# Kernel optimization log

Measured on AMD Instinct MI355X. Metric: run time of the kernel, lower is better.

Reference implementation:

```python
import jax, jax.numpy as jnp
import numpy as np
import itertools

F = 3          # num_sparse_features
C = 256        # num_categories
D = 64         # embedding_dim
H = 1024       # hidden_units
ND = 13        # num_dense_features
B = 16384      # batch
COMBOS = [c for r in range(2, F + 1) for c in itertools.combinations(range(F), r)]
WIDE_DIM = C * F + sum(C ** len(c) for c in COMBOS) + ND
DEEP_IN = F * D + ND


def setup_inputs() -> dict:
    key = jax.random.key(0)
    ks = jax.random.split(key, 12)
    sparse_inputs = jax.random.randint(ks[0], (B, F), 0, C, dtype=jnp.int32)
    dense_inputs = jax.random.normal(ks[1], (B, ND), dtype=jnp.float32)
    wide_w = jax.random.normal(ks[2], (WIDE_DIM,), dtype=jnp.float32) * 0.01
    wide_b = jax.random.normal(ks[3], (1,), dtype=jnp.float32) * 0.01
    emb = jax.random.normal(ks[4], (F, C, D), dtype=jnp.float32) * 0.05
    W1 = jax.random.normal(ks[5], (H, DEEP_IN), dtype=jnp.float32) / np.sqrt(DEEP_IN).astype(np.float32)
    b1 = jnp.zeros((H,), jnp.float32)
    W2 = jax.random.normal(ks[6], (H, H), dtype=jnp.float32) / np.sqrt(H).astype(np.float32)
    b2 = jnp.zeros((H,), jnp.float32)
    W3 = jax.random.normal(ks[7], (1, H), dtype=jnp.float32) / np.sqrt(H).astype(np.float32)
    b3 = jnp.zeros((1,), jnp.float32)
    return {"sparse_inputs": sparse_inputs, "dense_inputs": dense_inputs,
            "wide_w": wide_w, "wide_b": wide_b, "emb": emb,
            "W1": W1, "b1": b1, "W2": W2, "b2": b2, "W3": W3, "b3": b3}


def reference(sparse_inputs, dense_inputs, wide_w, wide_b, emb, W1, b1, W2, b2, W3, b3):
    # Wide path: one_hot(x) @ W.T  ==  gather of W columns at the hot indices.
    wide = wide_b[0]  # scalar, broadcasts to [B]
    for i in range(F):  # per-feature one-hot block, width C each
        wide = wide + wide_w[i * C + sparse_inputs[:, i]]
    off = F * C
    for combo in COMBOS:  # cross-feature one-hot blocks, width C**len(combo)
        cross = sparse_inputs[:, combo[0]]
        for j in combo[1:]:
            # faithful to source: multiplies by num_sparse_features (F), not C
            cross = cross * F + sparse_inputs[:, j]
        wide = wide + wide_w[off + cross]
        off += C ** len(combo)
    wide = wide + dense_inputs @ wide_w[off:off + ND]  # dense tail of wide linear
    wide = wide[:, None]  # [B, 1]

    # Deep path: per-feature embedding lookup -> concat -> 3-layer MLP
    embedded = jnp.concatenate([emb[i][sparse_inputs[:, i]] for i in range(F)], axis=1)  # [B, F*D]
    deep_x = jnp.concatenate([embedded, dense_inputs], axis=1)  # [B, DEEP_IN]
    h = jax.nn.relu(deep_x @ W1.T + b1)
    h = jax.nn.relu(h @ W2.T + b2)
    deep = h @ W3.T + b3  # [B, 1]

    return jax.nn.sigmoid(wide + deep)
```

## Files before the change

kernel.cpp:

```cpp
#include <hip/hip_runtime.h>
#include <stdint.h>


#define BATCH 16384
#define HDIM 1024
#define KPAD 256
#define DEEP_IN 205

typedef short bf16x8 __attribute__((ext_vector_type(8)));
typedef float f32x4 __attribute__((ext_vector_type(4)));
typedef uint16_t u16x8 __attribute__((ext_vector_type(8)));

__device__ __forceinline__ float bf2f(uint16_t u) {
    uint32_t x = ((uint32_t)u) << 16;
    float f;
    __builtin_memcpy(&f, &x, 4);
    return f;
}

__device__ __forceinline__ uint16_t f2bf(float f) {
    uint32_t x;
    __builtin_memcpy(&x, &f, 4);
    uint32_t r = (x + 0x7fffu + ((x >> 16) & 1u)) >> 16;
    return (uint16_t)r;
}

__device__ __forceinline__ void async_ld16(const uint16_t* g, uint16_t* l) {
    __builtin_amdgcn_global_load_lds(
        (const __attribute__((address_space(1))) uint32_t*)g,
        (__attribute__((address_space(3))) uint32_t*)l, 16, 0, 0);
}

__global__ __launch_bounds__(256) void prep_kernel(
    const int* __restrict__ sp, const float* __restrict__ dense,
    const float* __restrict__ emb,
    const float* __restrict__ W1, const float* __restrict__ W2,
    const float* __restrict__ ww, const float* __restrict__ wb,
    const float* __restrict__ b3,
    uint16_t* __restrict__ dx, uint16_t* __restrict__ W1b,
    uint16_t* __restrict__ W2b, float* __restrict__ wide)
{
    const int bid = blockIdx.x;
    if (bid < 2048) {
        int idx = bid * 256 + threadIdx.x;
        int b = idx >> 5, c0 = (idx & 31) * 8;
        u16x8 o;
        if (c0 < 192) {
            int f = c0 >> 6, cc = c0 & 63;
            int s = sp[b * 3 + f];
            const float* e = emb + (size_t)(((f << 8) + s) * 64 + cc);
            float4 v0 = *(const float4*)e;
            float4 v1 = *(const float4*)(e + 4);
            o[0] = f2bf(v0.x); o[1] = f2bf(v0.y); o[2] = f2bf(v0.z); o[3] = f2bf(v0.w);
            o[4] = f2bf(v1.x); o[5] = f2bf(v1.y); o[6] = f2bf(v1.z); o[7] = f2bf(v1.w);
        } else {
#pragma unroll
            for (int t = 0; t < 8; t++) {
                int c = c0 + t;
                o[t] = (c >= 192 && c < DEEP_IN) ? f2bf(dense[b * 13 + (c - 192)])
                                                 : (uint16_t)0;
            }
        }
        *(u16x8*)(dx + (size_t)idx * 8) = o;
    } else if (bid < 2560) {
        int k = (bid - 2048) * 256 + threadIdx.x;
        const float* src = W2 + (size_t)k * 8;
        float4 v0 = *(const float4*)src;
        float4 v1 = *(const float4*)(src + 4);
        u16x8 o;
        o[0] = f2bf(v0.x); o[1] = f2bf(v0.y); o[2] = f2bf(v0.z); o[3] = f2bf(v0.w);
        o[4] = f2bf(v1.x); o[5] = f2bf(v1.y); o[6] = f2bf(v1.z); o[7] = f2bf(v1.w);
        *(u16x8*)(W2b + (size_t)k * 8) = o;
    } else if (bid < 2688) {
        int idx = (bid - 2560) * 256 + threadIdx.x;
        int n = idx >> 5, c0 = (idx & 31) * 8;
        u16x8 o;
#pragma unroll
        for (int t = 0; t < 8; t++) {
            int c = c0 + t;
            o[t] = (c < DEEP_IN) ? f2bf(W1[n * DEEP_IN + c]) : (uint16_t)0;
        }
        *(u16x8*)(W1b + (size_t)idx * 8) = o;
    } else {
        int b = (bid - 2688) * 256 + threadIdx.x;
        int s0 = sp[b * 3], s1 = sp[b * 3 + 1], s2 = sp[b * 3 + 2];
        float w = wb[0] + b3[0];
        w += ww[s0] + ww[256 + s1] + ww[512 + s2];
        w += ww[768    + s0 * 3 + s1];
        w += ww[66304  + s0 * 3 + s2];
        w += ww[131840 + s1 * 3 + s2];
        w += ww[197376 + (s0 * 3 + s1) * 3 + s2];
        const float* wd = ww + 16974592;
        float acc = 0.f;
#pragma unroll
        for (int j = 0; j < 13; j++) acc += dense[b * 13 + j] * wd[j];
        wide[b] = w + acc;
    }
}

#define GEMM_CORE(A_, B_, K_)                                                  \
    const int tid = threadIdx.x;                                               \
    const int lane = tid & 63;                                                 \
    const int wave = tid >> 6;                                                 \
    const int wm = wave >> 2;                                                  \
    const int wn = wave & 3;                                                   \
    const int id = blockIdx.x;                                                 \
    const int xcd = id & 7;                                                    \
    const int slot = id >> 3;                                                  \
    const int mbX = (M >> 7) >> 3;                                             \
    const int by = xcd * mbX + (slot >> 2);                                    \
    const int bx = slot & 3;                                                   \
    const int bm = by * 128;                                                   \
    const int bn = bx * 256;                                                   \
    const int rl = lane & 15, q = lane >> 4;                                   \
    f32x4 acc[4][4];                                                           \
    _Pragma("unroll") for (int i = 0; i < 4; i++)                              \
        _Pragma("unroll") for (int j = 0; j < 4; j++) acc[i][j] = (f32x4)0.f;  \
    const uint16_t* aS = A_ + (size_t)(bm + wave * 16 + rl) * K_ + q * 8;      \
    const uint16_t* bS0 = B_ + (size_t)(bn + wave * 32 + rl) * K_ + q * 8;     \
    const uint16_t* bS1 = bS0 + (size_t)16 * K_;                               \
    const int dA = wave * 512, dB0 = wave * 1024, dB1 = wave * 1024 + 512;     \
    async_ld16(aS, &Al[0][dA]);                                                \
    async_ld16(bS0, &Bl[0][dB0]);                                              \
    async_ld16(bS1, &Bl[0][dB1]);                                              \
    asm volatile("s_waitcnt vmcnt(0)" ::: "memory");                           \
    __syncthreads();                                                           \
    int p = 0;                                                                 \
    for (int k0 = 32; k0 < K_; k0 += 32) {                                     \
        async_ld16(aS + k0, &Al[p ^ 1][dA]);                                   \
        async_ld16(bS0 + k0, &Bl[p ^ 1][dB0]);                                 \
        async_ld16(bS1 + k0, &Bl[p ^ 1][dB1]);                                 \
        bf16x8 af[4], bfr[4];                                                  \
        _Pragma("unroll") for (int i = 0; i < 4; i++)                          \
            af[i] = *(const bf16x8*)&Al[p][(wm * 4 + i) * 512 + lane * 8];     \
        _Pragma("unroll") for (int j = 0; j < 4; j++)                          \
            bfr[j] = *(const bf16x8*)&Bl[p][(wn * 4 + j) * 512 + lane * 8];    \
        _Pragma("unroll") for (int i = 0; i < 4; i++)                          \
            _Pragma("unroll") for (int j = 0; j < 4; j++)                      \
                acc[i][j] = __builtin_amdgcn_mfma_f32_16x16x32_bf16(           \
                    af[i], bfr[j], acc[i][j], 0, 0, 0);                        \
        asm volatile("s_waitcnt vmcnt(0)" ::: "memory");                       \
        __syncthreads();                                                       \
        p ^= 1;                                                                \
    }                                                                          \
    {                                                                          \
        bf16x8 af[4], bfr[4];                                                  \
        _Pragma("unroll") for (int i = 0; i < 4; i++)                          \
            af[i] = *(const bf16x8*)&Al[p][(wm * 4 + i) * 512 + lane * 8];     \
        _Pragma("unroll") for (int j = 0; j < 4; j++)                          \
            bfr[j] = *(const bf16x8*)&Bl[p][(wn * 4 + j) * 512 + lane * 8];    \
        _Pragma("unroll") for (int i = 0; i < 4; i++)                          \
            _Pragma("unroll") for (int j = 0; j < 4; j++)                      \
                acc[i][j] = __builtin_amdgcn_mfma_f32_16x16x32_bf16(           \
                    af[i], bfr[j], acc[i][j], 0, 0, 0);                        \
    }

__global__ __launch_bounds__(512, 4) void gemm_relu(
    const uint16_t* __restrict__ A, const uint16_t* __restrict__ Bw,
    const float* __restrict__ bias, uint16_t* __restrict__ C,
    int M, int N, int K)
{
    __shared__ __align__(16) uint16_t Al[2][4096];
    __shared__ __align__(16) uint16_t Bl[2][8192];
    GEMM_CORE(A, Bw, K)
#pragma unroll
    for (int i = 0; i < 4; i++) {
#pragma unroll
        for (int j = 0; j < 4; j++) {
            int n = bn + (wn * 4 + j) * 16 + rl;
            float bv = bias[n];
#pragma unroll
            for (int r = 0; r < 4; r++) {
                int m = bm + (wm * 4 + i) * 16 + q * 4 + r;
                float v = fmaxf(acc[i][j][r] + bv, 0.f);
                C[(size_t)m * N + n] = f2bf(v);
            }
        }
    }
}

__global__ __launch_bounds__(512, 4) void gemm_fused(
    const uint16_t* __restrict__ A, const uint16_t* __restrict__ Bw,
    const float* __restrict__ bias, const float* __restrict__ W3,
    float* __restrict__ outacc, int M, int N, int K)
{
    __shared__ __align__(16) uint16_t Al[2][4096];
    __shared__ __align__(16) uint16_t Bl[2][8192];
    GEMM_CORE(A, Bw, K)
    float bv[4], w3v[4];
#pragma unroll
    for (int j = 0; j < 4; j++) {
        int n = bn + (wn * 4 + j) * 16 + rl;
        bv[j] = bias[n];
        w3v[j] = W3[n];
    }
#pragma unroll
    for (int i = 0; i < 4; i++) {
#pragma unroll
        for (int r = 0; r < 4; r++) {
            float pt = 0.f;
#pragma unroll
            for (int j = 0; j < 4; j++)
                pt += fmaxf(acc[i][j][r] + bv[j], 0.f) * w3v[j];
            pt += __shfl_xor(pt, 1);
            pt += __shfl_xor(pt, 2);
            pt += __shfl_xor(pt, 4);
            pt += __shfl_xor(pt, 8);
            if (rl == 0) {
                int m = bm + (wm * 4 + i) * 16 + q * 4 + r;
                atomicAdd(&outacc[m], pt);
            }
        }
    }
}

__global__ __launch_bounds__(256) void sigmoid_kernel(
    const float* __restrict__ outacc, float* __restrict__ out)
{
    int b = blockIdx.x * 256 + threadIdx.x;
    out[b] = 1.f / (1.f + __expf(-outacc[b]));
}

extern "C" void kernel_launch(void* const* d_in, const int* in_sizes, int n_in,
                              void* d_out, int out_size, void* d_ws, size_t ws_size,
                              hipStream_t stream) {
    const int*   sp    = (const int*)d_in[0];
    const float* dense = (const float*)d_in[1];
    const float* ww    = (const float*)d_in[2];
    const float* wb    = (const float*)d_in[3];
    const float* emb   = (const float*)d_in[4];
    const float* W1    = (const float*)d_in[5];
    const float* b1    = (const float*)d_in[6];
    const float* W2    = (const float*)d_in[7];
    const float* b2    = (const float*)d_in[8];
    const float* W3    = (const float*)d_in[9];
    const float* b3    = (const float*)d_in[10];
    float* out = (float*)d_out;

    char* ws = (char*)d_ws;
    float*    wide = (float*)ws;
    uint16_t* dxp  = (uint16_t*)(ws + 65536);
    uint16_t* W1b  = (uint16_t*)(ws + 8454144);
    uint16_t* W2b  = (uint16_t*)(ws + 8978432);
    uint16_t* h1   = (uint16_t*)(ws + 11075584);

    prep_kernel<<<2752, 256, 0, stream>>>(sp, dense, emb, W1, W2, ww, wb, b3,
                                          dxp, W1b, W2b, wide);
    gemm_relu<<<(BATCH / 128) * 4, 512, 0, stream>>>(
        dxp, W1b, b1, h1, BATCH, HDIM, KPAD);
    gemm_fused<<<(BATCH / 128) * 4, 512, 0, stream>>>(
        h1, W2b, b2, W3, wide, BATCH, HDIM, HDIM);
    sigmoid_kernel<<<BATCH / 256, 256, 0, stream>>>(wide, out);
}
```

Before: 184.0 us.

## Switch GEMM core to triple-buffered LDS pipeline with one barrier per step

The GEMM main loop moves from double to triple buffering in shared memory. Each step waits with vmcnt(3), so the next tile's loads stay in flight, and uses a single s_barrier per iteration instead of a full drain plus barrier. Redundant wraparound prefetches are issued at the end so the loop stays uniform. The cost is 50% more LDS per block, which can lower occupancy, plus a few wasted loads in the last iterations.

```diff
diff --git a/kernel.cpp b/kernel.cpp
--- a/kernel.cpp
+++ b/kernel.cpp
@@ -120,48 +120,46 @@
     const uint16_t* bS0 = B_ + (size_t)(bn + wave * 32 + rl) * K_ + q * 8;     \
     const uint16_t* bS1 = bS0 + (size_t)16 * K_;                               \
     const int dA = wave * 512, dB0 = wave * 1024, dB1 = wave * 1024 + 512;     \
+    const int niter = (K_) >> 5;                                               \
+       \
     async_ld16(aS, &Al[0][dA]);                                                \
     async_ld16(bS0, &Bl[0][dB0]);                                              \
     async_ld16(bS1, &Bl[0][dB1]);                                              \
-    asm volatile("s_waitcnt vmcnt(0)" ::: "memory");                           \
-    __syncthreads();                                                           \
-    int p = 0;                                                                 \
-    for (int k0 = 32; k0 < K_; k0 += 32) {                                     \
-        async_ld16(aS + k0, &Al[p ^ 1][dA]);                                   \
-        async_ld16(bS0 + k0, &Bl[p ^ 1][dB0]);                                 \
-        async_ld16(bS1 + k0, &Bl[p ^ 1][dB1]);                                 \
+    async_ld16(aS + 32, &Al[1][dA]);                                           \
+    async_ld16(bS0 + 32, &Bl[1][dB0]);                                         \
+    async_ld16(bS1 + 32, &Bl[1][dB1]);                                         \
+    int pc = 0;                                              \
+    int k2 = 2;                     \
+    if (k2 >= niter) k2 -= niter;                                              \
+    for (int k = 0; k < niter; ++k) {                                          \
+        asm volatile("s_waitcnt vmcnt(3)" ::: "memory");                       \
+        asm volatile("s_barrier" ::: "memory");                                \
+        int pf = pc + 2; if (pf >= 3) pf -= 3;                                 \
+        const int ko = k2 << 5;                                                \
+        async_ld16(aS + ko, &Al[pf][dA]);                                      \
+        async_ld16(bS0 + ko, &Bl[pf][dB0]);                                    \
+        async_ld16(bS1 + ko, &Bl[pf][dB1]);                                    \
+        k2++; if (k2 >= niter) k2 = 0;                                         \
         bf16x8 af[4], bfr[4];                                                  \
         _Pragma("unroll") for (int i = 0; i < 4; i++)                          \
-            af[i] = *(const bf16x8*)&Al[p][(wm * 4 + i) * 512 + lane * 8];     \
+            af[i] = *(const bf16x8*)&Al[pc][(wm * 4 + i) * 512 + lane * 8];    \
         _Pragma("unroll") for (int j = 0; j < 4; j++)                          \
-            bfr[j] = *(const bf16x8*)&Bl[p][(wn * 4 + j) * 512 + lane * 8];    \
+            bfr[j] = *(const bf16x8*)&Bl[pc][(wn * 4 + j) * 512 + lane * 8];   \
         _Pragma("unroll") for (int i = 0; i < 4; i++)                          \
             _Pragma("unroll") for (int j = 0; j < 4; j++)                      \
                 acc[i][j] = __builtin_amdgcn_mfma_f32_16x16x32_bf16(           \
                     af[i], bfr[j], acc[i][j], 0, 0, 0);                        \
-        asm volatile("s_waitcnt vmcnt(0)" ::: "memory");                       \
-        __syncthreads();                                                       \
-        p ^= 1;                                                                \
+        pc++; if (pc >= 3) pc -= 3;                                            \
     }                                                                          \
-    {                                                                          \
-        bf16x8 af[4], bfr[4];                                                  \
-        _Pragma("unroll") for (int i = 0; i < 4; i++)                          \
-            af[i] = *(const bf16x8*)&Al[p][(wm * 4 + i) * 512 + lane * 8];     \
-        _Pragma("unroll") for (int j = 0; j < 4; j++)                          \
-            bfr[j] = *(const bf16x8*)&Bl[p][(wn * 4 + j) * 512 + lane * 8];    \
-        _Pragma("unroll") for (int i = 0; i < 4; i++)                          \
-            _Pragma("unroll") for (int j = 0; j < 4; j++)                      \
-                acc[i][j] = __builtin_amdgcn_mfma_f32_16x16x32_bf16(           \
-                    af[i], bfr[j], acc[i][j], 0, 0, 0);                        \
-    }
+    asm volatile("s_waitcnt vmcnt(0)" ::: "memory");
 
 __global__ __launch_bounds__(512, 4) void gemm_relu(
     const uint16_t* __restrict__ A, const uint16_t* __restrict__ Bw,
     const float* __restrict__ bias, uint16_t* __restrict__ C,
     int M, int N, int K)
 {
-    __shared__ __align__(16) uint16_t Al[2][4096];
-    __shared__ __align__(16) uint16_t Bl[2][8192];
+    __shared__ __align__(16) uint16_t Al[3][4096];
+    __shared__ __align__(16) uint16_t Bl[3][8192];
     GEMM_CORE(A, Bw, K)
 #pragma unroll
     for (int i = 0; i < 4; i++) {
@@ -184,8 +182,8 @@
     const float* __restrict__ bias, const float* __restrict__ W3,
     float* __restrict__ outacc, int M, int N, int K)
 {
-    __shared__ __align__(16) uint16_t Al[2][4096];
-    __shared__ __align__(16) uint16_t Bl[2][8192];
+    __shared__ __align__(16) uint16_t Al[3][4096];
+    __shared__ __align__(16) uint16_t Bl[3][8192];
     GEMM_CORE(A, Bw, K)
     float bv[4], w3v[4];
 #pragma unroll
```

New measurement: 190.0 us. 3.3% more time.

## Switch GEMMs to 32x32x16 MFMA tiles and trim first-layer K padding

Applied to the files above, without the earlier changes.

Replaces the 16x16x32 bf16 MFMA fragments with 32x32x16 MFMAs (2x2 accumulators of 16 floats per wave) and reworks the LDS staging layout and epilogue indexing to match. It also shrinks the padded K of the first layer from 256 to 224, which cuts both prep work and first-GEMM iterations. The larger MFMA gives more FLOPs per LDS fragment read and fewer instructions. The risk lies in the LDS fragment mapping and the output row indexing, which must match the 32x32 accumulator layout exactly.

```diff
diff --git a/kernel.cpp b/kernel.cpp
--- a/kernel.cpp
+++ b/kernel.cpp
@@ -4,19 +4,12 @@
 
 #define BATCH 16384
 #define HDIM 1024
-#define KPAD 256
+#define K1 224
 #define DEEP_IN 205
 
 typedef short bf16x8 __attribute__((ext_vector_type(8)));
-typedef float f32x4 __attribute__((ext_vector_type(4)));
+typedef float f32x16 __attribute__((ext_vector_type(16)));
 typedef uint16_t u16x8 __attribute__((ext_vector_type(8)));
-
-__device__ __forceinline__ float bf2f(uint16_t u) {
-    uint32_t x = ((uint32_t)u) << 16;
-    float f;
-    __builtin_memcpy(&f, &x, 4);
-    return f;
-}
 
 __device__ __forceinline__ uint16_t f2bf(float f) {
     uint32_t x;
@@ -41,9 +34,9 @@
     uint16_t* __restrict__ W2b, float* __restrict__ wide)
 {
     const int bid = blockIdx.x;
-    if (bid < 2048) {
+    if (bid < 1792) {
         int idx = bid * 256 + threadIdx.x;
-        int b = idx >> 5, c0 = (idx & 31) * 8;
+        int b = idx / 28, c0 = (idx - b * 28) * 8;
         u16x8 o;
         if (c0 < 192) {
             int f = c0 >> 6, cc = c0 & 63;
@@ -57,13 +50,13 @@
 #pragma unroll
             for (int t = 0; t < 8; t++) {
                 int c = c0 + t;
-                o[t] = (c >= 192 && c < DEEP_IN) ? f2bf(dense[b * 13 + (c - 192)])
-                                                 : (uint16_t)0;
+                o[t] = (c < DEEP_IN) ? f2bf(dense[b * 13 + (c - 192)])
+                                     : (uint16_t)0;
             }
         }
-        *(u16x8*)(dx + (size_t)idx * 8) = o;
-    } else if (bid < 2560) {
-        int k = (bid - 2048) * 256 + threadIdx.x;
+        *(u16x8*)(dx + (size_t)b * K1 + c0) = o;
+    } else if (bid < 2304) {
+        int k = (bid - 1792) * 256 + threadIdx.x;
         const float* src = W2 + (size_t)k * 8;
         float4 v0 = *(const float4*)src;
         float4 v1 = *(const float4*)(src + 4);
@@ -71,18 +64,18 @@
         o[0] = f2bf(v0.x); o[1] = f2bf(v0.y); o[2] = f2bf(v0.z); o[3] = f2bf(v0.w);
         o[4] = f2bf(v1.x); o[5] = f2bf(v1.y); o[6] = f2bf(v1.z); o[7] = f2bf(v1.w);
         *(u16x8*)(W2b + (size_t)k * 8) = o;
-    } else if (bid < 2688) {
-        int idx = (bid - 2560) * 256 + threadIdx.x;
-        int n = idx >> 5, c0 = (idx & 31) * 8;
+    } else if (bid < 2416) {
+        int idx = (bid - 2304) * 256 + threadIdx.x;
+        int n = idx / 28, c0 = (idx - n * 28) * 8;
         u16x8 o;
 #pragma unroll
         for (int t = 0; t < 8; t++) {
             int c = c0 + t;
             o[t] = (c < DEEP_IN) ? f2bf(W1[n * DEEP_IN + c]) : (uint16_t)0;
         }
-        *(u16x8*)(W1b + (size_t)idx * 8) = o;
+        *(u16x8*)(W1b + (size_t)n * K1 + c0) = o;
     } else {
-        int b = (bid - 2688) * 256 + threadIdx.x;
+        int b = (bid - 2416) * 256 + threadIdx.x;
         int s0 = sp[b * 3], s1 = sp[b * 3 + 1], s2 = sp[b * 3 + 2];
         float w = wb[0] + b3[0];
         w += ww[s0] + ww[256 + s1] + ww[512 + s2];
@@ -112,47 +105,62 @@
     const int bx = slot & 3;                                                   \
     const int bm = by * 128;                                                   \
     const int bn = bx * 256;                                                   \
-    const int rl = lane & 15, q = lane >> 4;                                   \
-    f32x4 acc[4][4];                                                           \
-    _Pragma("unroll") for (int i = 0; i < 4; i++)                              \
-        _Pragma("unroll") for (int j = 0; j < 4; j++) acc[i][j] = (f32x4)0.f;  \
-    const uint16_t* aS = A_ + (size_t)(bm + wave * 16 + rl) * K_ + q * 8;      \
-    const uint16_t* bS0 = B_ + (size_t)(bn + wave * 32 + rl) * K_ + q * 8;     \
-    const uint16_t* bS1 = bS0 + (size_t)16 * K_;                               \
-    const int dA = wave * 512, dB0 = wave * 1024, dB1 = wave * 1024 + 512;     \
+    const int rl32 = lane & 31, q2 = lane >> 5;                                \
+    f32x16 acc[2][2];                                                          \
+    _Pragma("unroll") for (int i = 0; i < 2; i++)                              \
+        _Pragma("unroll") for (int j = 0; j < 2; j++) acc[i][j] = (f32x16)0.f; \
+    const uint16_t* aS = A_ + (size_t)(bm + (wave >> 1) * 32 + rl32) * K_      \
+                            + (wave & 1) * 16 + q2 * 8;                        \
+    const uint16_t* bS = B_ + (size_t)(bn + wave * 32 + rl32) * K_ + q2 * 8;   \
+    const int dA = wave * 512;                                                 \
+    const int dB0 = (2 * wave) * 512, dB1 = (2 * wave + 1) * 512;              \
     async_ld16(aS, &Al[0][dA]);                                                \
-    async_ld16(bS0, &Bl[0][dB0]);                                              \
-    async_ld16(bS1, &Bl[0][dB1]);                                              \
+    async_ld16(bS, &Bl[0][dB0]);                                               \
+    async_ld16(bS + 16, &Bl[0][dB1]);                                          \
     asm volatile("s_waitcnt vmcnt(0)" ::: "memory");                           \
     __syncthreads();                                                           \
     int p = 0;                                                                 \
     for (int k0 = 32; k0 < K_; k0 += 32) {                                     \
         async_ld16(aS + k0, &Al[p ^ 1][dA]);                                   \
-        async_ld16(bS0 + k0, &Bl[p ^ 1][dB0]);                                 \
-        async_ld16(bS1 + k0, &Bl[p ^ 1][dB1]);                                 \
-        bf16x8 af[4], bfr[4];                                                  \
-        _Pragma("unroll") for (int i = 0; i < 4; i++)                          \
-            af[i] = *(const bf16x8*)&Al[p][(wm * 4 + i) * 512 + lane * 8];     \
-        _Pragma("unroll") for (int j = 0; j < 4; j++)                          \
-            bfr[j] = *(const bf16x8*)&Bl[p][(wn * 4 + j) * 512 + lane * 8];    \
-        _Pragma("unroll") for (int i = 0; i < 4; i++)                          \
-            _Pragma("unroll") for (int j = 0; j < 4; j++)                      \
-                acc[i][j] = __builtin_amdgcn_mfma_f32_16x16x32_bf16(           \
-                    af[i], bfr[j], acc[i][j], 0, 0, 0);                        \
+        async_ld16(bS + k0, &Bl[p ^ 1][dB0]);                                  \
+        async_ld16(bS + k0 + 16, &Bl[p ^ 1][dB1]);                             \
+        bf16x8 af[2][2], bfr[2][2];                                            \
+        _Pragma("unroll") for (int i = 0; i < 2; i++)                          \
+            _Pragma("unroll") for (int kc = 0; kc < 2; kc++)                   \
+                af[i][kc] = *(const bf16x8*)                                   \
+                    &Al[p][((wm * 2 + i) * 2 + kc) * 512 + lane * 8];          \
+        _Pragma("unroll") for (int j = 0; j < 2; j++)                          \
+            _Pragma("unroll") for (int kc = 0; kc < 2; kc++)                   \
+                bfr[j][kc] = *(const bf16x8*)                                  \
+                    &Bl[p][((wn * 2 + j) * 2 + kc) * 512 + lane * 8];          \
+        _Pragma("unroll") for (int i = 0; i < 2; i++)                          \
+            _Pragma("unroll") for (int j = 0; j < 2; j++) {                    \
+                acc[i][j] = __builtin_amdgcn_mfma_f32_32x32x16_bf16(           \
+                    af[i][0], bfr[j][0], acc[i][j], 0, 0, 0);                  \
+                acc[i][j] = __builtin_amdgcn_mfma_f32_32x32x16_bf16(           \
+                    af[i][1], bfr[j][1], acc[i][j], 0, 0, 0);                  \
+            }                                                                  \
         asm volatile("s_waitcnt vmcnt(0)" ::: "memory");                       \
         __syncthreads();                                                       \
         p ^= 1;                                                                \
     }                                                                          \
     {                                                                          \
-        bf16x8 af[4], bfr[4];                                                  \
-        _Pragma("unroll") for (int i = 0; i < 4; i++)                          \
-            af[i] = *(const bf16x8*)&Al[p][(wm * 4 + i) * 512 + lane * 8];     \
-        _Pragma("unroll") for (int j = 0; j < 4; j++)                          \
-            bfr[j] = *(const bf16x8*)&Bl[p][(wn * 4 + j) * 512 + lane * 8];    \
-        _Pragma("unroll") for (int i = 0; i < 4; i++)                          \
-            _Pragma("unroll") for (int j = 0; j < 4; j++)                      \
-                acc[i][j] = __builtin_amdgcn_mfma_f32_16x16x32_bf16(           \
-                    af[i], bfr[j], acc[i][j], 0, 0, 0);                        \
+        bf16x8 af[2][2], bfr[2][2];                                            \
+        _Pragma("unroll") for (int i = 0; i < 2; i++)                          \
+            _Pragma("unroll") for (int kc = 0; kc < 2; kc++)                   \
+                af[i][kc] = *(const bf16x8*)                                   \
+                    &Al[p][((wm * 2 + i) * 2 + kc) * 512 + lane * 8];          \
+        _Pragma("unroll") for (int j = 0; j < 2; j++)                          \
+            _Pragma("unroll") for (int kc = 0; kc < 2; kc++)                   \
+                bfr[j][kc] = *(const bf16x8*)                                  \
+                    &Bl[p][((wn * 2 + j) * 2 + kc) * 512 + lane * 8];          \
+        _Pragma("unroll") for (int i = 0; i < 2; i++)                          \
+            _Pragma("unroll") for (int j = 0; j < 2; j++) {                    \
+                acc[i][j] = __builtin_amdgcn_mfma_f32_32x32x16_bf16(           \
+                    af[i][0], bfr[j][0], acc[i][j], 0, 0, 0);                  \
+                acc[i][j] = __builtin_amdgcn_mfma_f32_32x32x16_bf16(           \
+                    af[i][1], bfr[j][1], acc[i][j], 0, 0, 0);                  \
+            }                                                                  \
     }
 
 __global__ __launch_bounds__(512, 4) void gemm_relu(
@@ -164,14 +172,14 @@
     __shared__ __align__(16) uint16_t Bl[2][8192];
     GEMM_CORE(A, Bw, K)
 #pragma unroll
-    for (int i = 0; i < 4; i++) {
-#pragma unroll
-        for (int j = 0; j < 4; j++) {
-            int n = bn + (wn * 4 + j) * 16 + rl;
+    for (int i = 0; i < 2; i++) {
+#pragma unroll
+        for (int j = 0; j < 2; j++) {
+            int n = bn + (wn * 2 + j) * 32 + rl32;
             float bv = bias[n];
 #pragma unroll
-            for (int r = 0; r < 4; r++) {
-                int m = bm + (wm * 4 + i) * 16 + q * 4 + r;
+            for (int r = 0; r < 16; r++) {
+                int m = bm + (wm * 2 + i) * 32 + (r & 3) + 8 * (r >> 2) + 4 * q2;
                 float v = fmaxf(acc[i][j][r] + bv, 0.f);
                 C[(size_t)m * N + n] = f2bf(v);
             }
@@ -187,27 +195,28 @@
     __shared__ __align__(16) uint16_t Al[2][4096];
     __shared__ __align__(16) uint16_t Bl[2][8192];
     GEMM_CORE(A, Bw, K)
-    float bv[4], w3v[4];
-#pragma unroll
-    for (int j = 0; j < 4; j++) {
-        int n = bn + (wn * 4 + j) * 16 + rl;
+    float bv[2], w3v[2];
+#pragma unroll
+    for (int j = 0; j < 2; j++) {
+        int n = bn + (wn * 2 + j) * 32 + rl32;
         bv[j] = bias[n];
         w3v[j] = W3[n];
     }
 #pragma unroll
-    for (int i = 0; i < 4; i++) {
-#pragma unroll
-        for (int r = 0; r < 4; r++) {
+    for (int i = 0; i < 2; i++) {
+#pragma unroll
+        for (int r = 0; r < 16; r++) {
             float pt = 0.f;
 #pragma unroll
-            for (int j = 0; j < 4; j++)
+            for (int j = 0; j < 2; j++)
                 pt += fmaxf(acc[i][j][r] + bv[j], 0.f) * w3v[j];
             pt += __shfl_xor(pt, 1);
             pt += __shfl_xor(pt, 2);
             pt += __shfl_xor(pt, 4);
             pt += __shfl_xor(pt, 8);
-            if (rl == 0) {
-                int m = bm + (wm * 4 + i) * 16 + q * 4 + r;
+            pt += __shfl_xor(pt, 16);
+            if (rl32 == 0) {
+                int m = bm + (wm * 2 + i) * 32 + (r & 3) + 8 * (r >> 2) + 4 * q2;
                 atomicAdd(&outacc[m], pt);
             }
         }
@@ -240,14 +249,14 @@
     char* ws = (char*)d_ws;
     float*    wide = (float*)ws;
     uint16_t* dxp  = (uint16_t*)(ws + 65536);
-    uint16_t* W1b  = (uint16_t*)(ws + 8454144);
-    uint16_t* W2b  = (uint16_t*)(ws + 8978432);
-    uint16_t* h1   = (uint16_t*)(ws + 11075584);
-
-    prep_kernel<<<2752, 256, 0, stream>>>(sp, dense, emb, W1, W2, ww, wb, b3,
+    uint16_t* W1b  = (uint16_t*)(ws + 7405568);
+    uint16_t* W2b  = (uint16_t*)(ws + 7864320);
+    uint16_t* h1   = (uint16_t*)(ws + 9961472);
+
+    prep_kernel<<<2480, 256, 0, stream>>>(sp, dense, emb, W1, W2, ww, wb, b3,
                                           dxp, W1b, W2b, wide);
     gemm_relu<<<(BATCH / 128) * 4, 512, 0, stream>>>(
-        dxp, W1b, b1, h1, BATCH, HDIM, KPAD);
+        dxp, W1b, b1, h1, BATCH, HDIM, K1);
     gemm_fused<<<(BATCH / 128) * 4, 512, 0, stream>>>(
         h1, W2b, b2, W3, wide, BATCH, HDIM, HDIM);
     sigmoid_kernel<<<BATCH / 256, 256, 0, stream>>>(wide, out);
```

New measurement: 186.1 us. Within noise of the previous version (+1.1%).

## Trim layer-1 K padding, fold W2/wide prep into GEMM1, vectorize stores

Applied to the files above, without the earlier changes.

Reduces the padded K of the first GEMM from 256 to 224, which cuts the activation and W1 conversion traffic and skips one k-step. The W2 bf16 conversion and the wide-path computation move out of the prep kernel into extra blocks of the first GEMM launch, so they overlap with GEMM work. The B-operand column mapping is permuted so each lane owns 4 adjacent output columns, letting the relu epilogue write 4 bf16 values per store instead of scalar stores. The extra non-GEMM blocks add imbalance to the GEMM grid, and the permuted column mapping must stay consistent across both GEMMs.

```diff
diff --git a/kernel.cpp b/kernel.cpp
--- a/kernel.cpp
+++ b/kernel.cpp
@@ -4,19 +4,13 @@
 
 #define BATCH 16384
 #define HDIM 1024
-#define KPAD 256
+#define K1 224
 #define DEEP_IN 205
 
 typedef short bf16x8 __attribute__((ext_vector_type(8)));
 typedef float f32x4 __attribute__((ext_vector_type(4)));
 typedef uint16_t u16x8 __attribute__((ext_vector_type(8)));
-
-__device__ __forceinline__ float bf2f(uint16_t u) {
-    uint32_t x = ((uint32_t)u) << 16;
-    float f;
-    __builtin_memcpy(&f, &x, 4);
-    return f;
-}
+typedef uint16_t u16x4 __attribute__((ext_vector_type(4)));
 
 __device__ __forceinline__ uint16_t f2bf(float f) {
     uint32_t x;
@@ -33,17 +27,13 @@
 
 __global__ __launch_bounds__(256) void prep_kernel(
     const int* __restrict__ sp, const float* __restrict__ dense,
-    const float* __restrict__ emb,
-    const float* __restrict__ W1, const float* __restrict__ W2,
-    const float* __restrict__ ww, const float* __restrict__ wb,
-    const float* __restrict__ b3,
-    uint16_t* __restrict__ dx, uint16_t* __restrict__ W1b,
-    uint16_t* __restrict__ W2b, float* __restrict__ wide)
+    const float* __restrict__ emb, const float* __restrict__ W1,
+    uint16_t* __restrict__ dx, uint16_t* __restrict__ W1b)
 {
     const int bid = blockIdx.x;
-    if (bid < 2048) {
+    if (bid < 1792) {
         int idx = bid * 256 + threadIdx.x;
-        int b = idx >> 5, c0 = (idx & 31) * 8;
+        int b = idx / 28, c0 = (idx - b * 28) * 8;
         u16x8 o;
         if (c0 < 192) {
             int f = c0 >> 6, cc = c0 & 63;
@@ -57,54 +47,29 @@
 #pragma unroll
             for (int t = 0; t < 8; t++) {
                 int c = c0 + t;
-                o[t] = (c >= 192 && c < DEEP_IN) ? f2bf(dense[b * 13 + (c - 192)])
-                                                 : (uint16_t)0;
+                o[t] = (c < DEEP_IN) ? f2bf(dense[b * 13 + (c - 192)])
+                                     : (uint16_t)0;
             }
         }
-        *(u16x8*)(dx + (size_t)idx * 8) = o;
-    } else if (bid < 2560) {
-        int k = (bid - 2048) * 256 + threadIdx.x;
-        const float* src = W2 + (size_t)k * 8;
-        float4 v0 = *(const float4*)src;
-        float4 v1 = *(const float4*)(src + 4);
-        u16x8 o;
-        o[0] = f2bf(v0.x); o[1] = f2bf(v0.y); o[2] = f2bf(v0.z); o[3] = f2bf(v0.w);
-        o[4] = f2bf(v1.x); o[5] = f2bf(v1.y); o[6] = f2bf(v1.z); o[7] = f2bf(v1.w);
-        *(u16x8*)(W2b + (size_t)k * 8) = o;
-    } else if (bid < 2688) {
-        int idx = (bid - 2560) * 256 + threadIdx.x;
-        int n = idx >> 5, c0 = (idx & 31) * 8;
+        *(u16x8*)(dx + (size_t)b * K1 + c0) = o;
+    } else {
+        int idx = (bid - 1792) * 256 + threadIdx.x;
+        int n = idx / 28, c0 = (idx - n * 28) * 8;
         u16x8 o;
 #pragma unroll
         for (int t = 0; t < 8; t++) {
             int c = c0 + t;
             o[t] = (c < DEEP_IN) ? f2bf(W1[n * DEEP_IN + c]) : (uint16_t)0;
         }
-        *(u16x8*)(W1b + (size_t)idx * 8) = o;
-    } else {
-        int b = (bid - 2688) * 256 + threadIdx.x;
-        int s0 = sp[b * 3], s1 = sp[b * 3 + 1], s2 = sp[b * 3 + 2];
-        float w = wb[0] + b3[0];
-        w += ww[s0] + ww[256 + s1] + ww[512 + s2];
-        w += ww[768    + s0 * 3 + s1];
-        w += ww[66304  + s0 * 3 + s2];
-        w += ww[131840 + s1 * 3 + s2];
-        w += ww[197376 + (s0 * 3 + s1) * 3 + s2];
-        const float* wd = ww + 16974592;
-        float acc = 0.f;
-#pragma unroll
-        for (int j = 0; j < 13; j++) acc += dense[b * 13 + j] * wd[j];
-        wide[b] = w + acc;
+        *(u16x8*)(W1b + (size_t)n * K1 + c0) = o;
     }
 }
 
 #define GEMM_CORE(A_, B_, K_)                                                  \
-    const int tid = threadIdx.x;                                               \
     const int lane = tid & 63;                                                 \
     const int wave = tid >> 6;                                                 \
     const int wm = wave >> 2;                                                  \
     const int wn = wave & 3;                                                   \
-    const int id = blockIdx.x;                                                 \
     const int xcd = id & 7;                                                    \
     const int slot = id >> 3;                                                  \
     const int mbX = (M >> 7) >> 3;                                             \
@@ -116,10 +81,11 @@
     f32x4 acc[4][4];                                                           \
     _Pragma("unroll") for (int i = 0; i < 4; i++)                              \
         _Pragma("unroll") for (int j = 0; j < 4; j++) acc[i][j] = (f32x4)0.f;  \
+    const int c0 = 2 * wave, c1 = 2 * wave + 1;                                \
     const uint16_t* aS = A_ + (size_t)(bm + wave * 16 + rl) * K_ + q * 8;      \
-    const uint16_t* bS0 = B_ + (size_t)(bn + wave * 32 + rl) * K_ + q * 8;     \
-    const uint16_t* bS1 = bS0 + (size_t)16 * K_;                               \
-    const int dA = wave * 512, dB0 = wave * 1024, dB1 = wave * 1024 + 512;     \
+    const uint16_t* bS0 = B_ + (size_t)(bn + (c0 >> 2) * 64 + 4 * rl + (c0 & 3)) * K_ + q * 8; \
+    const uint16_t* bS1 = B_ + (size_t)(bn + (c1 >> 2) * 64 + 4 * rl + (c1 & 3)) * K_ + q * 8; \
+    const int dA = wave * 512, dB0 = c0 * 512, dB1 = c1 * 512;                 \
     async_ld16(aS, &Al[0][dA]);                                                \
     async_ld16(bS0, &Bl[0][dB0]);                                              \
     async_ld16(bS1, &Bl[0][dB1]);                                              \
@@ -158,23 +124,60 @@
 __global__ __launch_bounds__(512, 4) void gemm_relu(
     const uint16_t* __restrict__ A, const uint16_t* __restrict__ Bw,
     const float* __restrict__ bias, uint16_t* __restrict__ C,
+    const float* __restrict__ W2, uint16_t* __restrict__ W2b,
+    const int* __restrict__ sp, const float* __restrict__ dense,
+    const float* __restrict__ ww, const float* __restrict__ wb,
+    const float* __restrict__ b3, float* __restrict__ wide,
     int M, int N, int K)
 {
+    const int id = blockIdx.x;
+    const int tid = threadIdx.x;
+
+    if (id >= 512) {
+        if (id < 768) {
+            int k = (id - 512) * 512 + tid;
+            const float* src = W2 + (size_t)k * 8;
+            float4 v0 = *(const float4*)src;
+            float4 v1 = *(const float4*)(src + 4);
+            u16x8 o;
+            o[0] = f2bf(v0.x); o[1] = f2bf(v0.y); o[2] = f2bf(v0.z); o[3] = f2bf(v0.w);
+            o[4] = f2bf(v1.x); o[5] = f2bf(v1.y); o[6] = f2bf(v1.z); o[7] = f2bf(v1.w);
+            *(u16x8*)(W2b + (size_t)k * 8) = o;
+        } else {
+            int b = (id - 768) * 512 + tid;
+            int s0 = sp[b * 3], s1 = sp[b * 3 + 1], s2 = sp[b * 3 + 2];
+            float w = wb[0] + b3[0];
+            w += ww[s0] + ww[256 + s1] + ww[512 + s2];
+            w += ww[768    + s0 * 3 + s1];
+            w += ww[66304  + s0 * 3 + s2];
+            w += ww[131840 + s1 * 3 + s2];
+            w += ww[197376 + (s0 * 3 + s1) * 3 + s2];
+            const float* wd = ww + 16974592;
+            float acc2 = 0.f;
+#pragma unroll
+            for (int j = 0; j < 13; j++) acc2 += dense[b * 13 + j] * wd[j];
+            wide[b] = w + acc2;
+        }
+        return;
+    }
+
     __shared__ __align__(16) uint16_t Al[2][4096];
     __shared__ __align__(16) uint16_t Bl[2][8192];
     GEMM_CORE(A, Bw, K)
+
+    float bv[4];
+#pragma unroll
+    for (int j = 0; j < 4; j++) bv[j] = bias[bn + wn * 64 + 4 * rl + j];
 #pragma unroll
     for (int i = 0; i < 4; i++) {
 #pragma unroll
-        for (int j = 0; j < 4; j++) {
-            int n = bn + (wn * 4 + j) * 16 + rl;
-            float bv = bias[n];
-#pragma unroll
-            for (int r = 0; r < 4; r++) {
-                int m = bm + (wm * 4 + i) * 16 + q * 4 + r;
-                float v = fmaxf(acc[i][j][r] + bv, 0.f);
-                C[(size_t)m * N + n] = f2bf(v);
-            }
+        for (int r = 0; r < 4; r++) {
+            int m = bm + wm * 64 + i * 16 + q * 4 + r;
+            u16x4 o;
+#pragma unroll
+            for (int j = 0; j < 4; j++)
+                o[j] = f2bf(fmaxf(acc[i][j][r] + bv[j], 0.f));
+            *(u16x4*)&C[(size_t)m * N + bn + wn * 64 + 4 * rl] = o;
         }
     }
 }
@@ -184,13 +187,16 @@
     const float* __restrict__ bias, const float* __restrict__ W3,
     float* __restrict__ outacc, int M, int N, int K)
 {
+    const int id = blockIdx.x;
+    const int tid = threadIdx.x;
     __shared__ __align__(16) uint16_t Al[2][4096];
     __shared__ __align__(16) uint16_t Bl[2][8192];
     GEMM_CORE(A, Bw, K)
+
     float bv[4], w3v[4];
 #pragma unroll
     for (int j = 0; j < 4; j++) {
-        int n = bn + (wn * 4 + j) * 16 + rl;
+        int n = bn + wn * 64 + 4 * rl + j;
         bv[j] = bias[n];
         w3v[j] = W3[n];
     }
@@ -207,7 +213,7 @@
             pt += __shfl_xor(pt, 4);
             pt += __shfl_xor(pt, 8);
             if (rl == 0) {
-                int m = bm + (wm * 4 + i) * 16 + q * 4 + r;
+                int m = bm + wm * 64 + i * 16 + q * 4 + r;
                 atomicAdd(&outacc[m], pt);
             }
         }
@@ -240,14 +246,14 @@
     char* ws = (char*)d_ws;
     float*    wide = (float*)ws;
     uint16_t* dxp  = (uint16_t*)(ws + 65536);
-    uint16_t* W1b  = (uint16_t*)(ws + 8454144);
-    uint16_t* W2b  = (uint16_t*)(ws + 8978432);
-    uint16_t* h1   = (uint16_t*)(ws + 11075584);
-
-    prep_kernel<<<2752, 256, 0, stream>>>(sp, dense, emb, W1, W2, ww, wb, b3,
-                                          dxp, W1b, W2b, wide);
-    gemm_relu<<<(BATCH / 128) * 4, 512, 0, stream>>>(
-        dxp, W1b, b1, h1, BATCH, HDIM, KPAD);
+    uint16_t* W1b  = (uint16_t*)(ws + 7405568);
+    uint16_t* W2b  = (uint16_t*)(ws + 7864320);
+    uint16_t* h1   = (uint16_t*)(ws + 9961472);
+
+    prep_kernel<<<1904, 256, 0, stream>>>(sp, dense, emb, W1, dxp, W1b);
+    gemm_relu<<<800, 512, 0, stream>>>(
+        dxp, W1b, b1, h1, W2, W2b, sp, dense, ww, wb, b3, wide,
+        BATCH, HDIM, K1);
     gemm_fused<<<(BATCH / 128) * 4, 512, 0, stream>>>(
         h1, W2b, b2, W3, wide, BATCH, HDIM, HDIM);
     sigmoid_kernel<<<BATCH / 256, 256, 0, stream>>>(wide, out);
```

Result: no change. 181.9 us (-1.2%).
